# Optimization experiments

Hardware: AMD Instinct MI355X
Metric: run time of the kernel (lower is better)

## Reference

```python
import jax, jax.numpy as jnp
import numpy as np

N = 50000          # num nodes
E = 800000         # num edges (avg degree 16)
IN_C, HID_C, OUT_C = 128, 128, 64
LPA_ITER = 5


def setup_inputs() -> dict:
    key = jax.random.key(0)
    ks = jax.random.split(key, 8)
    x = jax.random.normal(ks[0], (N, IN_C), dtype=jnp.float32)
    soft_labels = jax.random.uniform(ks[1], (N, OUT_C), dtype=jnp.float32)
    edge_index = jax.random.randint(ks[2], (2, E), 0, N, dtype=jnp.int64)
    # learnable edge weights: abs() in the original, so keep them positive
    edge_attr = jax.random.uniform(ks[3], (E,), dtype=jnp.float32, minval=0.1, maxval=1.0)
    # GCNConv params (lin weight + bias)
    w1 = jax.random.normal(ks[4], (IN_C, HID_C), dtype=jnp.float32) / np.sqrt(IN_C)
    b1 = jnp.zeros((HID_C,), dtype=jnp.float32)
    w2 = jax.random.normal(ks[5], (HID_C, OUT_C), dtype=jnp.float32) / np.sqrt(HID_C)
    b2 = jnp.zeros((OUT_C,), dtype=jnp.float32)
    return {"x": x, "soft_labels": soft_labels, "edge_attr": edge_attr,
            "w1": w1, "b1": b1, "w2": w2, "b2": b2, "edge_index": edge_index}


def reference(x, soft_labels, edge_attr, w1, b1, w2, b2, edge_index):
    row, col = edge_index[0], edge_index[1]
    n = x.shape[0]
    # row-normalize the weighted sparse adjacency: A_n = D^{-1} A
    deg = jax.ops.segment_sum(edge_attr, row, num_segments=n)  # [N]
    deg_inv = jnp.where(deg == 0, 0.0, 1.0 / deg)              # inf -> 0
    val = deg_inv[row] * edge_attr                              # [E]

    def spmm(v):  # A_n @ v,  v: [N, F]
        return jax.ops.segment_sum(val[:, None] * v[col], row, num_segments=n)

    # eval mode: dropout(p=0.5, training=False) is identity
    h = jax.nn.relu(spmm(x @ w1) + b1)        # GCNConv 1 (normalize=False)
    logits = spmm(h @ w2) + b2                # GCNConv 2
    x_out = jax.nn.sigmoid(logits)

    labels = soft_labels
    for _ in range(LPA_ITER):                 # label propagation
        labels = spmm(labels)
    labels = jax.nn.sigmoid(labels)
    return (x_out, labels)
```

## Files before the change

### kernel.cpp

```cpp
#include <hip/hip_runtime.h>
#include <cstdint>
#include <cstddef>


#define WS_ALIGN(x) (((x) + 255) & ~((size_t)255))

typedef __attribute__((ext_vector_type(8))) short short8;
typedef __attribute__((ext_vector_type(4))) float floatx4;

__device__ __forceinline__ unsigned short f2bf(float f) {
    unsigned u = __float_as_uint(f);
    u += 0x7fffu + ((u >> 16) & 1u);
    return (unsigned short)(u >> 16);
}
__device__ __forceinline__ float bf_lo(unsigned u) { return __uint_as_float(u << 16); }
__device__ __forceinline__ float bf_hi(unsigned u) { return __uint_as_float(u & 0xffff0000u); }
__device__ __forceinline__ float bf2f(unsigned short h) {
    return __uint_as_float(((unsigned)h) << 16);
}
__device__ __forceinline__ unsigned pack_bf2(float a, float b) {
    return (unsigned)f2bf(a) | ((unsigned)f2bf(b) << 16);
}
__device__ __forceinline__ float sigmoidf(float x) {
    return 1.f / (1.f + __expf(-x));
}
__device__ __forceinline__ int2 ld_nt_int2(const int2* p) {
    long long v = __builtin_nontemporal_load((const long long*)p);
    int2 r;
    r.x = (int)(unsigned)(v & 0xffffffffLL);
    r.y = (int)(v >> 32);
    return r;
}

static const int NBLK = 256;
#define MAXNB 256

__launch_bounds__(256)
__global__ void binA_count(const int* __restrict__ row, int* __restrict__ bucket_count,
                           int* __restrict__ bases, int E, int chunk, int NB)
{
    __shared__ int hist[MAXNB];
    const int t = threadIdx.x;
    const int blk = blockIdx.x;
    if (t < NB) hist[t] = 0;
    __syncthreads();
    const int s = blk * chunk;
    const int e = min(E, s + chunk);
    for (int i = s + t; i < e; i += 256)
        atomicAdd(&hist[row[i] >> 8], 1);
    __syncthreads();
    if (t < NB)
        bases[blk * NB + t] = atomicAdd(&bucket_count[t], hist[t]);
}

__launch_bounds__(256)
__global__ void bin_scan(const int* __restrict__ bucket_count, int* __restrict__ bucket_start,
                         int NB)
{
    __shared__ int s[256];
    const int t = threadIdx.x;
    int v = (t < NB) ? bucket_count[t] : 0;
    s[t] = v;
    __syncthreads();
    for (int off = 1; off < 256; off <<= 1) {
        int u = (t >= off) ? s[t - off] : 0;
        __syncthreads();
        s[t] += u;
        __syncthreads();
    }
    int excl = s[t] - v;
    if (t <= NB) bucket_start[t] = excl;
}

__launch_bounds__(256)
__global__ void binA_scatter(const int* __restrict__ row, const int* __restrict__ colv,
                             const float* __restrict__ ea,
                             const int* __restrict__ bucket_start, const int* __restrict__ bases,
                             int2* __restrict__ bk, int E, int chunk, int NB)
{
    __shared__ int cur[MAXNB];
    const int t = threadIdx.x;
    const int blk = blockIdx.x;
    if (t < NB) cur[t] = bucket_start[t] + bases[blk * NB + t];
    __syncthreads();
    const int s = blk * chunk;
    const int e = min(E, s + chunk);
    for (int i = s + t; i < e; i += 256) {
        int r = row[i];
        int bin = r >> 8;
        int pos = atomicAdd(&cur[bin], 1);
        bk[pos] = make_int2(((r & 255) << 16) | colv[i], __float_as_int(ea[i]));
    }
}

__launch_bounds__(256)
__global__ void binB(const int2* __restrict__ bk, const int* __restrict__ bucket_start,
                     int* __restrict__ rowptr, int2* __restrict__ edges, int N)
{
    __shared__ int cnt[256];
    __shared__ float deg[256];
    __shared__ float inv[256];
    __shared__ int excl_s[256];
    __shared__ int cur[256];
    __shared__ int scantmp[256];
    const int b = blockIdx.x;
    const int t = threadIdx.x;
    const int s = bucket_start[b];
    const int e = bucket_start[b + 1];
    cnt[t] = 0;
    deg[t] = 0.f;
    __syncthreads();
    for (int i = s + t; i < e; i += 256) {
        int2 v = bk[i];
        int rl = ((unsigned)v.x) >> 16;
        atomicAdd(&cnt[rl], 1);
        atomicAdd(&deg[rl], __int_as_float(v.y));
    }
    __syncthreads();
    const int myc = cnt[t];
    scantmp[t] = myc;
    __syncthreads();
    for (int off = 1; off < 256; off <<= 1) {
        int u = (t >= off) ? scantmp[t - off] : 0;
        __syncthreads();
        scantmp[t] += u;
        __syncthreads();
    }
    const int excl = scantmp[t] - myc;
    excl_s[t] = excl;
    float d = deg[t];
    inv[t] = (d > 0.f) ? 1.f / d : 0.f;
    cur[t] = 0;
    const int gr = b * 256 + t;
    if (gr <= N) rowptr[gr] = s + excl;
    __syncthreads();
    for (int i = s + t; i < e; i += 256) {
        int2 v = bk[i];
        int rl = ((unsigned)v.x) >> 16;
        int c = v.x & 0xffff;
        int p = s + excl_s[rl] + atomicAdd(&cur[rl], 1);
        edges[p] = make_int2(c, __float_as_int(__int_as_float(v.y) * inv[rl]));
    }
}

__global__ void f32_to_bf16_kernel(const float* __restrict__ in, unsigned short* __restrict__ out,
                                   int n2)
{
    int i = blockIdx.x * 256 + threadIdx.x;
    if (i < n2) {
        float2 v = ((const float2*)in)[i];
        ((unsigned*)out)[i] = pack_bf2(v.x, v.y);
    }
}

template<int COLS>
__global__ void pack_w_kernel(const float* __restrict__ W, unsigned short* __restrict__ Wp)
{
    const int total = (COLS / 16) * 4 * 64;
    int idx = blockIdx.x * 256 + threadIdx.x;
    if (idx >= total) return;
    const int l = idx & 63;
    const int t = (idx >> 6) & 3;
    const int ct = idx >> 8;
    const int kbase = t * 32 + (l >> 4) * 8;
    const int col = ct * 16 + (l & 15);
    unsigned short v[8];
#pragma unroll
    for (int j = 0; j < 8; ++j)
        v[j] = f2bf(W[(size_t)(kbase + j) * COLS + col]);
    uint4 o;
    o.x = (unsigned)v[0] | ((unsigned)v[1] << 16);
    o.y = (unsigned)v[2] | ((unsigned)v[3] << 16);
    o.z = (unsigned)v[4] | ((unsigned)v[5] << 16);
    o.w = (unsigned)v[6] | ((unsigned)v[7] << 16);
    *(uint4*)(Wp + (size_t)idx * 8) = o;
}

template<int COLS>
__launch_bounds__(256)
__global__ void gemm_mfma_f32a(const float* __restrict__ A,
                               const unsigned short* __restrict__ Wp,
                               unsigned short* __restrict__ C, int M)
{
    const int wave = threadIdx.x >> 6;
    const int lane = threadIdx.x & 63;
    const int row0 = blockIdx.x * 64 + wave * 16;
    const int m = lane & 15;
    const int q = lane >> 4;

    const int arow = row0 + m;
    const bool avalid = arow < M;
    short8 a[4];
#pragma unroll
    for (int t = 0; t < 4; ++t) {
        if (avalid) {
            float4 f0 = *(const float4*)(A + (size_t)arow * 128 + t * 32 + q * 8);
            float4 f1 = *(const float4*)(A + (size_t)arow * 128 + t * 32 + q * 8 + 4);
            a[t][0] = (short)f2bf(f0.x); a[t][1] = (short)f2bf(f0.y);
            a[t][2] = (short)f2bf(f0.z); a[t][3] = (short)f2bf(f0.w);
            a[t][4] = (short)f2bf(f1.x); a[t][5] = (short)f2bf(f1.y);
            a[t][6] = (short)f2bf(f1.z); a[t][7] = (short)f2bf(f1.w);
        } else {
            a[t] = (short8)0;
        }
    }

#pragma unroll
    for (int ct = 0; ct < COLS / 16; ++ct) {
        floatx4 acc = {0.f, 0.f, 0.f, 0.f};
#pragma unroll
        for (int t = 0; t < 4; ++t) {
            short8 b = *(const short8*)(Wp + (size_t)((ct * 4 + t) * 64 + lane) * 8);
            acc = __builtin_amdgcn_mfma_f32_16x16x32_bf16(a[t], b, acc, 0, 0, 0);
        }
        const int col = ct * 16 + m;
#pragma unroll
        for (int r = 0; r < 4; ++r) {
            int orow = row0 + q * 4 + r;
            if (orow < M)
                C[(size_t)orow * COLS + col] = f2bf(acc[r]);
        }
    }
}

template<int COLS>
__launch_bounds__(256)
__global__ void gemm_mfma(const unsigned short* __restrict__ A,
                          const unsigned short* __restrict__ Wp,
                          unsigned short* __restrict__ C, int M)
{
    const int wave = threadIdx.x >> 6;
    const int lane = threadIdx.x & 63;
    const int row0 = blockIdx.x * 64 + wave * 16;
    const int m = lane & 15;
    const int q = lane >> 4;

    const int arow = row0 + m;
    const bool avalid = arow < M;
    short8 a[4];
#pragma unroll
    for (int t = 0; t < 4; ++t) {
        if (avalid)
            a[t] = *(const short8*)(A + (size_t)arow * 128 + t * 32 + q * 8);
        else
            a[t] = (short8)0;
    }

#pragma unroll
    for (int ct = 0; ct < COLS / 16; ++ct) {
        floatx4 acc = {0.f, 0.f, 0.f, 0.f};
#pragma unroll
        for (int t = 0; t < 4; ++t) {
            short8 b = *(const short8*)(Wp + (size_t)((ct * 4 + t) * 64 + lane) * 8);
            acc = __builtin_amdgcn_mfma_f32_16x16x32_bf16(a[t], b, acc, 0, 0, 0);
        }
        const int col = ct * 16 + m;
#pragma unroll
        for (int r = 0; r < 4; ++r) {
            int orow = row0 + q * 4 + r;
            if (orow < M)
                C[(size_t)orow * COLS + col] = f2bf(acc[r]);
        }
    }
}

__launch_bounds__(256)
__global__ void fused1_pair(const int* __restrict__ rowptr, const int2* __restrict__ edges,
                            const uint2* __restrict__ srcA,
                            const unsigned* __restrict__ srcB,
                            const float* __restrict__ bias,
                            uint2* __restrict__ outA,
                            unsigned* __restrict__ outB,
                            int n)
{
    const int row = blockIdx.x * 4 + (threadIdx.x >> 6);
    const int lane = threadIdx.x & 63;
    const int f = lane & 31;
    const int half = lane >> 5;
    if (row >= n) return;
    const int s = rowptr[row];
    const int e = rowptr[row + 1];

    float a0[4], a1[4], b0[2], b1[2];
#pragma unroll
    for (int j = 0; j < 4; ++j) { a0[j] = 0.f; a1[j] = 0.f; }
    b0[0] = b0[1] = b1[0] = b1[1] = 0.f;

    int i = s;
    for (; i + 8 <= e; i += 8) {
        int2 ed[4]; uint2 ua[4]; unsigned ub[4];
#pragma unroll
        for (int j = 0; j < 4; ++j) ed[j] = ld_nt_int2(&edges[i + 2 * j + half]);
#pragma unroll
        for (int j = 0; j < 4; ++j) ua[j] = srcA[(size_t)ed[j].x * 32 + f];
#pragma unroll
        for (int j = 0; j < 4; ++j) ub[j] = srcB[(size_t)ed[j].x * 32 + f];
#pragma unroll
        for (int j = 0; j < 4; ++j) {
            float w = __int_as_float(ed[j].y);
            float* A = (j & 1) ? a1 : a0;
            float* B = (j & 1) ? b1 : b0;
            A[0] = fmaf(w, bf_lo(ua[j].x), A[0]);
            A[1] = fmaf(w, bf_hi(ua[j].x), A[1]);
            A[2] = fmaf(w, bf_lo(ua[j].y), A[2]);
            A[3] = fmaf(w, bf_hi(ua[j].y), A[3]);
            B[0] = fmaf(w, bf_lo(ub[j]), B[0]);
            B[1] = fmaf(w, bf_hi(ub[j]), B[1]);
        }
    }
    for (; i + 2 <= e; i += 2) {
        int2 ed = ld_nt_int2(&edges[i + half]);
        float w = __int_as_float(ed.y);
        uint2 ua = srcA[(size_t)ed.x * 32 + f];
        unsigned ub = srcB[(size_t)ed.x * 32 + f];
        a0[0] = fmaf(w, bf_lo(ua.x), a0[0]);
        a0[1] = fmaf(w, bf_hi(ua.x), a0[1]);
        a0[2] = fmaf(w, bf_lo(ua.y), a0[2]);
        a0[3] = fmaf(w, bf_hi(ua.y), a0[3]);
        b0[0] = fmaf(w, bf_lo(ub), b0[0]);
        b0[1] = fmaf(w, bf_hi(ub), b0[1]);
    }
    if (i < e && half == 0) {
        int2 ed = ld_nt_int2(&edges[i]);
        float w = __int_as_float(ed.y);
        uint2 ua = srcA[(size_t)ed.x * 32 + f];
        unsigned ub = srcB[(size_t)ed.x * 32 + f];
        a1[0] = fmaf(w, bf_lo(ua.x), a1[0]);
        a1[1] = fmaf(w, bf_hi(ua.x), a1[1]);
        a1[2] = fmaf(w, bf_lo(ua.y), a1[2]);
        a1[3] = fmaf(w, bf_hi(ua.y), a1[3]);
        b1[0] = fmaf(w, bf_lo(ub), b1[0]);
        b1[1] = fmaf(w, bf_hi(ub), b1[1]);
    }
    float A0 = a0[0] + a1[0], A1 = a0[1] + a1[1];
    float A2 = a0[2] + a1[2], A3 = a0[3] + a1[3];
    float B0 = b0[0] + b1[0], B1 = b0[1] + b1[1];
    A0 += __shfl_down(A0, 32); A1 += __shfl_down(A1, 32);
    A2 += __shfl_down(A2, 32); A3 += __shfl_down(A3, 32);
    B0 += __shfl_down(B0, 32); B1 += __shfl_down(B1, 32);
    if (half == 0) {
        float4 bb = *(const float4*)(bias + 4 * f);
        A0 = fmaxf(A0 + bb.x, 0.f);
        A1 = fmaxf(A1 + bb.y, 0.f);
        A2 = fmaxf(A2 + bb.z, 0.f);
        A3 = fmaxf(A3 + bb.w, 0.f);
        uint2 o;
        o.x = pack_bf2(A0, A1);
        o.y = pack_bf2(A2, A3);
        outA[(size_t)row * 32 + f] = o;
        outB[(size_t)row * 32 + f] = pack_bf2(B0, B1);
    }
}

__launch_bounds__(256)
__global__ void fused2_pair(const int* __restrict__ rowptr, const int2* __restrict__ edges,
                            const unsigned* __restrict__ srcA,
                            const unsigned* __restrict__ srcB,
                            const float* __restrict__ bias,
                            float* __restrict__ outA,
                            unsigned* __restrict__ outB,
                            int n)
{
    const int row = blockIdx.x * 4 + (threadIdx.x >> 6);
    const int lane = threadIdx.x & 63;
    const int f = lane & 31;
    const int half = lane >> 5;
    if (row >= n) return;
    const int s = rowptr[row];
    const int e = rowptr[row + 1];

    float a0[2], a1[2], b0[2], b1[2];
    a0[0] = a0[1] = a1[0] = a1[1] = 0.f;
    b0[0] = b0[1] = b1[0] = b1[1] = 0.f;

    int i = s;
    for (; i + 8 <= e; i += 8) {
        int2 ed[4]; unsigned ua[4], ub[4];
#pragma unroll
        for (int j = 0; j < 4; ++j) ed[j] = ld_nt_int2(&edges[i + 2 * j + half]);
#pragma unroll
        for (int j = 0; j < 4; ++j) ua[j] = srcA[(size_t)ed[j].x * 32 + f];
#pragma unroll
        for (int j = 0; j < 4; ++j) ub[j] = srcB[(size_t)ed[j].x * 32 + f];
#pragma unroll
        for (int j = 0; j < 4; ++j) {
            float w = __int_as_float(ed[j].y);
            float* A = (j & 1) ? a1 : a0;
            float* B = (j & 1) ? b1 : b0;
            A[0] = fmaf(w, bf_lo(ua[j]), A[0]);
            A[1] = fmaf(w, bf_hi(ua[j]), A[1]);
            B[0] = fmaf(w, bf_lo(ub[j]), B[0]);
            B[1] = fmaf(w, bf_hi(ub[j]), B[1]);
        }
    }
    for (; i + 2 <= e; i += 2) {
        int2 ed = ld_nt_int2(&edges[i + half]);
        float w = __int_as_float(ed.y);
        unsigned ua = srcA[(size_t)ed.x * 32 + f];
        unsigned ub = srcB[(size_t)ed.x * 32 + f];
        a0[0] = fmaf(w, bf_lo(ua), a0[0]);
        a0[1] = fmaf(w, bf_hi(ua), a0[1]);
        b0[0] = fmaf(w, bf_lo(ub), b0[0]);
        b0[1] = fmaf(w, bf_hi(ub), b0[1]);
    }
    if (i < e && half == 0) {
        int2 ed = ld_nt_int2(&edges[i]);
        float w = __int_as_float(ed.y);
        unsigned ua = srcA[(size_t)ed.x * 32 + f];
        unsigned ub = srcB[(size_t)ed.x * 32 + f];
        a1[0] = fmaf(w, bf_lo(ua), a1[0]);
        a1[1] = fmaf(w, bf_hi(ua), a1[1]);
        b1[0] = fmaf(w, bf_lo(ub), b1[0]);
        b1[1] = fmaf(w, bf_hi(ub), b1[1]);
    }
    float A0 = a0[0] + a1[0], A1 = a0[1] + a1[1];
    float B0 = b0[0] + b1[0], B1 = b0[1] + b1[1];
    A0 += __shfl_down(A0, 32); A1 += __shfl_down(A1, 32);
    B0 += __shfl_down(B0, 32); B1 += __shfl_down(B1, 32);
    if (half == 0) {
        float2 bb = *(const float2*)(bias + 2 * f);
        float2 o;
        o.x = sigmoidf(A0 + bb.x);
        o.y = sigmoidf(A1 + bb.y);
        *(float2*)(outA + (size_t)row * 64 + 2 * f) = o;
        outB[(size_t)row * 32 + f] = pack_bf2(B0, B1);
    }
}

template<int ACT>
__launch_bounds__(256)
__global__ void spmm64_pair(const int* __restrict__ rowptr, const int2* __restrict__ edges,
                            const unsigned* __restrict__ src,
                            void* __restrict__ out, int n)
{
    const int row = blockIdx.x * 4 + (threadIdx.x >> 6);
    const int lane = threadIdx.x & 63;
    const int f = lane & 31;
    const int half = lane >> 5;
    if (row >= n) return;
    const int s = rowptr[row];
    const int e = rowptr[row + 1];

    float a[4][2];
#pragma unroll
    for (int j = 0; j < 4; ++j) { a[j][0] = 0.f; a[j][1] = 0.f; }

    int i = s;
    for (; i + 8 <= e; i += 8) {
        int2 ed[4]; unsigned u[4];
#pragma unroll
        for (int j = 0; j < 4; ++j) ed[j] = ld_nt_int2(&edges[i + 2 * j + half]);
#pragma unroll
        for (int j = 0; j < 4; ++j) u[j] = src[(size_t)ed[j].x * 32 + f];
#pragma unroll
        for (int j = 0; j < 4; ++j) {
            float w = __int_as_float(ed[j].y);
            a[j][0] = fmaf(w, bf_lo(u[j]), a[j][0]);
            a[j][1] = fmaf(w, bf_hi(u[j]), a[j][1]);
        }
    }
    for (; i + 2 <= e; i += 2) {
        int2 ed = ld_nt_int2(&edges[i + half]);
        float w = __int_as_float(ed.y);
        unsigned u = src[(size_t)ed.x * 32 + f];
        a[0][0] = fmaf(w, bf_lo(u), a[0][0]);
        a[0][1] = fmaf(w, bf_hi(u), a[0][1]);
    }
    if (i < e && half == 0) {
        int2 ed = ld_nt_int2(&edges[i]);
        float w = __int_as_float(ed.y);
        unsigned u = src[(size_t)ed.x * 32 + f];
        a[1][0] = fmaf(w, bf_lo(u), a[1][0]);
        a[1][1] = fmaf(w, bf_hi(u), a[1][1]);
    }
    float v0 = (a[0][0] + a[1][0]) + (a[2][0] + a[3][0]);
    float v1 = (a[0][1] + a[1][1]) + (a[2][1] + a[3][1]);
    v0 += __shfl_down(v0, 32);
    v1 += __shfl_down(v1, 32);
    if (half == 0) {
        if (ACT == 0) {
            ((unsigned*)out)[(size_t)row * 32 + f] = pack_bf2(v0, v1);
        } else {
            float2 o;
            o.x = sigmoidf(v0);
            o.y = sigmoidf(v1);
            *(float2*)((float*)out + (size_t)row * 64 + 2 * f) = o;
        }
    }
}

extern "C" void kernel_launch(void* const* d_in, const int* in_sizes, int n_in,
                              void* d_out, int out_size, void* d_ws, size_t ws_size,
                              hipStream_t stream)
{
    const float* x    = (const float*)d_in[0];
    const float* soft = (const float*)d_in[1];
    const float* ea   = (const float*)d_in[2];
    const float* w1   = (const float*)d_in[3];
    const float* b1   = (const float*)d_in[4];
    const float* w2   = (const float*)d_in[5];
    const float* b2   = (const float*)d_in[6];
    const int*   eidx = (const int*)d_in[7];

    const int N = in_sizes[0] / 128;
    const int E = in_sizes[2];
    const int* row  = eidx;
    const int* colv = eidx + E;
    const int NB = (N + 255) / 256;
    const int chunk = (E + NBLK - 1) / NBLK;

    uint8_t* ws = (uint8_t*)d_ws;
    size_t off = 0;
    auto alloc = [&](size_t bytes) -> void* {
        void* p = ws + off;
        off += WS_ALIGN(bytes);
        return p;
    };
    int*  bucket_count = (int*) alloc((size_t)NB * 4);
    int*  bucket_start = (int*) alloc(((size_t)NB + 1) * 4);
    int*  bases        = (int*) alloc((size_t)NBLK * NB * 4);
    int*  rowptr       = (int*) alloc(((size_t)N + 1) * 4);
    int2* bk           = (int2*)alloc((size_t)E * 8);
    int2* edges        = (int2*)alloc((size_t)E * 8);
    unsigned short* w1p     = (unsigned short*)alloc((size_t)128 * 128 * 2);
    unsigned short* w2p     = (unsigned short*)alloc((size_t)128 * 64 * 2);
    unsigned short* xw1b    = (unsigned short*)alloc((size_t)N * 128 * 2);
    unsigned short* hb      = (unsigned short*)alloc((size_t)N * 128 * 2);
    unsigned short* logitsb = (unsigned short*)alloc((size_t)N * 64 * 2);
    unsigned short* softb   = (unsigned short*)alloc((size_t)N * 64 * 2);
    unsigned short* labA    = (unsigned short*)alloc((size_t)N * 64 * 2);
    unsigned short* labB    = (unsigned short*)alloc((size_t)N * 64 * 2);

    float* out0 = (float*)d_out;
    float* out1 = out0 + (size_t)N * 64;

    hipMemsetAsync(bucket_count, 0, (size_t)NB * 4, stream);

    binA_count<<<NBLK, 256, 0, stream>>>(row, bucket_count, bases, E, chunk, NB);
    bin_scan<<<1, 256, 0, stream>>>(bucket_count, bucket_start, NB);
    binA_scatter<<<NBLK, 256, 0, stream>>>(row, colv, ea, bucket_start, bases, bk, E, chunk, NB);
    binB<<<NB, 256, 0, stream>>>(bk, bucket_start, rowptr, edges, N);

    const int ns2 = (N * 64) / 2;
    f32_to_bf16_kernel<<<(ns2 + 255) / 256, 256, 0, stream>>>(soft, softb, ns2);
    pack_w_kernel<128><<<8, 256, 0, stream>>>(w1, w1p);
    pack_w_kernel<64><<<4, 256, 0, stream>>>(w2, w2p);

    const int gGemm = (N + 63) / 64;
    const int gSp   = (N + 3) / 4;

    gemm_mfma_f32a<128><<<gGemm, 256, 0, stream>>>(x, w1p, xw1b, N);

    fused1_pair<<<gSp, 256, 0, stream>>>(rowptr, edges, (const uint2*)xw1b,
                                         (const unsigned*)softb, b1,
                                         (uint2*)hb, (unsigned*)labA, N);

    gemm_mfma<64><<<gGemm, 256, 0, stream>>>(hb, w2p, logitsb, N);

    fused2_pair<<<gSp, 256, 0, stream>>>(rowptr, edges, (const unsigned*)logitsb,
                                         (const unsigned*)labA, b2,
                                         out0, (unsigned*)labB, N);

    spmm64_pair<0><<<gSp, 256, 0, stream>>>(rowptr, edges, (const unsigned*)labB, labA, N);
    spmm64_pair<0><<<gSp, 256, 0, stream>>>(rowptr, edges, (const unsigned*)labA, labB, N);
    spmm64_pair<3><<<gSp, 256, 0, stream>>>(rowptr, edges, (const unsigned*)labB, out1, N);
}
```

Measured before the change: 317.8 us.

## Split each row's wave into four edge lanes with wider gathers and merge prep kernels

The SpMM kernels now split each 64-lane wave into four 16-lane groups, each handling a different edge. Each lane gathers 8 or 16 bytes per feature row instead of 4 or 8, and each group loads two edges with a single 16-byte nontemporal load. Partial sums are reduced with two xor-shuffles. This is meant to cut the number of gather instructions and raise memory-level parallelism per wave, at the cost of more registers and extra shuffle work. The three small prep launches (soft-label bf16 conversion and the two weight packs) are merged into one kernel to save launch overhead. The edge buffer gets padding so the paired load cannot read past the end.

Measured after the change: 323.2 us. No clear change (+1.7%).

```diff
diff --git a/kernel.cpp b/kernel.cpp
--- a/kernel.cpp
+++ b/kernel.cpp
@@ -7,6 +7,7 @@
 
 typedef __attribute__((ext_vector_type(8))) short short8;
 typedef __attribute__((ext_vector_type(4))) float floatx4;
+typedef __attribute__((ext_vector_type(4))) int intx4;
 
 __device__ __forceinline__ unsigned short f2bf(float f) {
     unsigned u = __float_as_uint(f);
@@ -15,9 +16,6 @@
 }
 __device__ __forceinline__ float bf_lo(unsigned u) { return __uint_as_float(u << 16); }
 __device__ __forceinline__ float bf_hi(unsigned u) { return __uint_as_float(u & 0xffff0000u); }
-__device__ __forceinline__ float bf2f(unsigned short h) {
-    return __uint_as_float(((unsigned)h) << 16);
-}
 __device__ __forceinline__ unsigned pack_bf2(float a, float b) {
     return (unsigned)f2bf(a) | ((unsigned)f2bf(b) << 16);
 }
@@ -30,6 +28,10 @@
     r.x = (int)(unsigned)(v & 0xffffffffLL);
     r.y = (int)(v >> 32);
     return r;
+}
+struct __attribute__((packed, aligned(8))) intx4_a8 { intx4 v; };
+__device__ __forceinline__ intx4 ld_nt_edge2(const int2* p) {
+    return __builtin_nontemporal_load(&((const intx4_a8*)p)->v);
 }
 
 static const int NBLK = 256;
@@ -143,21 +145,11 @@
     }
 }
 
-__global__ void f32_to_bf16_kernel(const float* __restrict__ in, unsigned short* __restrict__ out,
-                                   int n2)
-{
-    int i = blockIdx.x * 256 + threadIdx.x;
-    if (i < n2) {
-        float2 v = ((const float2*)in)[i];
-        ((unsigned*)out)[i] = pack_bf2(v.x, v.y);
-    }
-}
-
 template<int COLS>
-__global__ void pack_w_kernel(const float* __restrict__ W, unsigned short* __restrict__ Wp)
+__device__ __forceinline__ void pack_w_body(const float* __restrict__ W,
+                                            unsigned short* __restrict__ Wp, int idx)
 {
     const int total = (COLS / 16) * 4 * 64;
-    int idx = blockIdx.x * 256 + threadIdx.x;
     if (idx >= total) return;
     const int l = idx & 63;
     const int t = (idx >> 6) & 3;
@@ -174,6 +166,27 @@
     o.z = (unsigned)v[4] | ((unsigned)v[5] << 16);
     o.w = (unsigned)v[6] | ((unsigned)v[7] << 16);
     *(uint4*)(Wp + (size_t)idx * 8) = o;
+}
+
+__launch_bounds__(256)
+__global__ void prep_kernel(const float* __restrict__ soft, unsigned short* __restrict__ softb,
+                            int ns2,
+                            const float* __restrict__ w1, unsigned short* __restrict__ w1p,
+                            const float* __restrict__ w2, unsigned short* __restrict__ w2p)
+{
+    const int b = blockIdx.x;
+    const int t = threadIdx.x;
+    if (b < 8) {
+        pack_w_body<128>(w1, w1p, b * 256 + t);
+    } else if (b < 12) {
+        pack_w_body<64>(w2, w2p, (b - 8) * 256 + t);
+    } else {
+        int i = (b - 12) * 256 + t;
+        if (i < ns2) {
+            float2 v = ((const float2*)soft)[i];
+            ((unsigned*)softb)[i] = pack_bf2(v.x, v.y);
+        }
+    }
 }
 
 template<int COLS>
@@ -265,226 +278,240 @@
 }
 
 __launch_bounds__(256)
-__global__ void fused1_pair(const int* __restrict__ rowptr, const int2* __restrict__ edges,
-                            const uint2* __restrict__ srcA,
-                            const unsigned* __restrict__ srcB,
+__global__ void fused1_quad(const int* __restrict__ rowptr, const int2* __restrict__ edges,
+                            const uint4* __restrict__ srcA,
+                            const uint2* __restrict__ srcB,
                             const float* __restrict__ bias,
-                            uint2* __restrict__ outA,
-                            unsigned* __restrict__ outB,
+                            uint4* __restrict__ outA,
+                            uint2* __restrict__ outB,
                             int n)
 {
     const int row = blockIdx.x * 4 + (threadIdx.x >> 6);
     const int lane = threadIdx.x & 63;
-    const int f = lane & 31;
-    const int half = lane >> 5;
+    const int f = lane & 15;
+    const int q = lane >> 4;
     if (row >= n) return;
     const int s = rowptr[row];
     const int e = rowptr[row + 1];
 
-    float a0[4], a1[4], b0[2], b1[2];
-#pragma unroll
-    for (int j = 0; j < 4; ++j) { a0[j] = 0.f; a1[j] = 0.f; }
-    b0[0] = b0[1] = b1[0] = b1[1] = 0.f;
+    float A0[8], A1[8], B0[4], B1[4];
+#pragma unroll
+    for (int k = 0; k < 8; ++k) { A0[k] = 0.f; A1[k] = 0.f; }
+#pragma unroll
+    for (int k = 0; k < 4; ++k) { B0[k] = 0.f; B1[k] = 0.f; }
 
     int i = s;
     for (; i + 8 <= e; i += 8) {
-        int2 ed[4]; uint2 ua[4]; unsigned ub[4];
-#pragma unroll
-        for (int j = 0; j < 4; ++j) ed[j] = ld_nt_int2(&edges[i + 2 * j + half]);
-#pragma unroll
-        for (int j = 0; j < 4; ++j) ua[j] = srcA[(size_t)ed[j].x * 32 + f];
-#pragma unroll
-        for (int j = 0; j < 4; ++j) ub[j] = srcB[(size_t)ed[j].x * 32 + f];
-#pragma unroll
-        for (int j = 0; j < 4; ++j) {
-            float w = __int_as_float(ed[j].y);
-            float* A = (j & 1) ? a1 : a0;
-            float* B = (j & 1) ? b1 : b0;
-            A[0] = fmaf(w, bf_lo(ua[j].x), A[0]);
-            A[1] = fmaf(w, bf_hi(ua[j].x), A[1]);
-            A[2] = fmaf(w, bf_lo(ua[j].y), A[2]);
-            A[3] = fmaf(w, bf_hi(ua[j].y), A[3]);
-            B[0] = fmaf(w, bf_lo(ub[j]), B[0]);
-            B[1] = fmaf(w, bf_hi(ub[j]), B[1]);
-        }
-    }
-    for (; i + 2 <= e; i += 2) {
-        int2 ed = ld_nt_int2(&edges[i + half]);
-        float w = __int_as_float(ed.y);
-        uint2 ua = srcA[(size_t)ed.x * 32 + f];
-        unsigned ub = srcB[(size_t)ed.x * 32 + f];
-        a0[0] = fmaf(w, bf_lo(ua.x), a0[0]);
-        a0[1] = fmaf(w, bf_hi(ua.x), a0[1]);
-        a0[2] = fmaf(w, bf_lo(ua.y), a0[2]);
-        a0[3] = fmaf(w, bf_hi(ua.y), a0[3]);
-        b0[0] = fmaf(w, bf_lo(ub), b0[0]);
-        b0[1] = fmaf(w, bf_hi(ub), b0[1]);
-    }
-    if (i < e && half == 0) {
-        int2 ed = ld_nt_int2(&edges[i]);
-        float w = __int_as_float(ed.y);
-        uint2 ua = srcA[(size_t)ed.x * 32 + f];
-        unsigned ub = srcB[(size_t)ed.x * 32 + f];
-        a1[0] = fmaf(w, bf_lo(ua.x), a1[0]);
-        a1[1] = fmaf(w, bf_hi(ua.x), a1[1]);
-        a1[2] = fmaf(w, bf_lo(ua.y), a1[2]);
-        a1[3] = fmaf(w, bf_hi(ua.y), a1[3]);
-        b1[0] = fmaf(w, bf_lo(ub), b1[0]);
-        b1[1] = fmaf(w, bf_hi(ub), b1[1]);
-    }
-    float A0 = a0[0] + a1[0], A1 = a0[1] + a1[1];
-    float A2 = a0[2] + a1[2], A3 = a0[3] + a1[3];
-    float B0 = b0[0] + b1[0], B1 = b0[1] + b1[1];
-    A0 += __shfl_down(A0, 32); A1 += __shfl_down(A1, 32);
-    A2 += __shfl_down(A2, 32); A3 += __shfl_down(A3, 32);
-    B0 += __shfl_down(B0, 32); B1 += __shfl_down(B1, 32);
-    if (half == 0) {
-        float4 bb = *(const float4*)(bias + 4 * f);
-        A0 = fmaxf(A0 + bb.x, 0.f);
-        A1 = fmaxf(A1 + bb.y, 0.f);
-        A2 = fmaxf(A2 + bb.z, 0.f);
-        A3 = fmaxf(A3 + bb.w, 0.f);
-        uint2 o;
-        o.x = pack_bf2(A0, A1);
-        o.y = pack_bf2(A2, A3);
-        outA[(size_t)row * 32 + f] = o;
-        outB[(size_t)row * 32 + f] = pack_bf2(B0, B1);
-    }
-}
-
-__launch_bounds__(256)
-__global__ void fused2_pair(const int* __restrict__ rowptr, const int2* __restrict__ edges,
-                            const unsigned* __restrict__ srcA,
-                            const unsigned* __restrict__ srcB,
+        intx4 ed = ld_nt_edge2(&edges[i + 2 * q]);
+        int c0 = ed.x, c1 = ed.z;
+        float wg0 = __int_as_float(ed.y);
+        float wg1 = __int_as_float(ed.w);
+        uint4 ua0 = srcA[c0 * 16 + f];
+        uint4 ua1 = srcA[c1 * 16 + f];
+        uint2 ub0 = srcB[c0 * 16 + f];
+        uint2 ub1 = srcB[c1 * 16 + f];
+        A0[0] = fmaf(wg0, bf_lo(ua0.x), A0[0]); A0[1] = fmaf(wg0, bf_hi(ua0.x), A0[1]);
+        A0[2] = fmaf(wg0, bf_lo(ua0.y), A0[2]); A0[3] = fmaf(wg0, bf_hi(ua0.y), A0[3]);
+        A0[4] = fmaf(wg0, bf_lo(ua0.z), A0[4]); A0[5] = fmaf(wg0, bf_hi(ua0.z), A0[5]);
+        A0[6] = fmaf(wg0, bf_lo(ua0.w), A0[6]); A0[7] = fmaf(wg0, bf_hi(ua0.w), A0[7]);
+        A1[0] = fmaf(wg1, bf_lo(ua1.x), A1[0]); A1[1] = fmaf(wg1, bf_hi(ua1.x), A1[1]);
+        A1[2] = fmaf(wg1, bf_lo(ua1.y), A1[2]); A1[3] = fmaf(wg1, bf_hi(ua1.y), A1[3]);
+        A1[4] = fmaf(wg1, bf_lo(ua1.z), A1[4]); A1[5] = fmaf(wg1, bf_hi(ua1.z), A1[5]);
+        A1[6] = fmaf(wg1, bf_lo(ua1.w), A1[6]); A1[7] = fmaf(wg1, bf_hi(ua1.w), A1[7]);
+        B0[0] = fmaf(wg0, bf_lo(ub0.x), B0[0]); B0[1] = fmaf(wg0, bf_hi(ub0.x), B0[1]);
+        B0[2] = fmaf(wg0, bf_lo(ub0.y), B0[2]); B0[3] = fmaf(wg0, bf_hi(ub0.y), B0[3]);
+        B1[0] = fmaf(wg1, bf_lo(ub1.x), B1[0]); B1[1] = fmaf(wg1, bf_hi(ub1.x), B1[1]);
+        B1[2] = fmaf(wg1, bf_lo(ub1.y), B1[2]); B1[3] = fmaf(wg1, bf_hi(ub1.y), B1[3]);
+    }
+#pragma unroll
+    for (int tslot = 0; tslot < 2; ++tslot) {
+        int idx = i + q + tslot * 4;
+        if (idx < e) {
+            int2 ed = ld_nt_int2(&edges[idx]);
+            float wg = __int_as_float(ed.y);
+            uint4 ua = srcA[ed.x * 16 + f];
+            uint2 ub = srcB[ed.x * 16 + f];
+            float* A = tslot ? A1 : A0;
+            float* B = tslot ? B1 : B0;
+            A[0] = fmaf(wg, bf_lo(ua.x), A[0]); A[1] = fmaf(wg, bf_hi(ua.x), A[1]);
+            A[2] = fmaf(wg, bf_lo(ua.y), A[2]); A[3] = fmaf(wg, bf_hi(ua.y), A[3]);
+            A[4] = fmaf(wg, bf_lo(ua.z), A[4]); A[5] = fmaf(wg, bf_hi(ua.z), A[5]);
+            A[6] = fmaf(wg, bf_lo(ua.w), A[6]); A[7] = fmaf(wg, bf_hi(ua.w), A[7]);
+            B[0] = fmaf(wg, bf_lo(ub.x), B[0]); B[1] = fmaf(wg, bf_hi(ub.x), B[1]);
+            B[2] = fmaf(wg, bf_lo(ub.y), B[2]); B[3] = fmaf(wg, bf_hi(ub.y), B[3]);
+        }
+    }
+#pragma unroll
+    for (int k = 0; k < 8; ++k) {
+        float v = A0[k] + A1[k];
+        v += __shfl_xor(v, 16);
+        v += __shfl_xor(v, 32);
+        A0[k] = v;
+    }
+#pragma unroll
+    for (int k = 0; k < 4; ++k) {
+        float v = B0[k] + B1[k];
+        v += __shfl_xor(v, 16);
+        v += __shfl_xor(v, 32);
+        B0[k] = v;
+    }
+    if (q == 0) {
+        float4 bb0 = *(const float4*)(bias + 8 * f);
+        float4 bb1 = *(const float4*)(bias + 8 * f + 4);
+        float h0 = fmaxf(A0[0] + bb0.x, 0.f), h1 = fmaxf(A0[1] + bb0.y, 0.f);
+        float h2 = fmaxf(A0[2] + bb0.z, 0.f), h3 = fmaxf(A0[3] + bb0.w, 0.f);
+        float h4 = fmaxf(A0[4] + bb1.x, 0.f), h5 = fmaxf(A0[5] + bb1.y, 0.f);
+        float h6 = fmaxf(A0[6] + bb1.z, 0.f), h7 = fmaxf(A0[7] + bb1.w, 0.f);
+        uint4 o;
+        o.x = pack_bf2(h0, h1);
+        o.y = pack_bf2(h2, h3);
+        o.z = pack_bf2(h4, h5);
+        o.w = pack_bf2(h6, h7);
+        outA[row * 16 + f] = o;
+        outB[row * 16 + f] = make_uint2(pack_bf2(B0[0], B0[1]), pack_bf2(B0[2], B0[3]));
+    }
+}
+
+__launch_bounds__(256)
+__global__ void fused2_quad(const int* __restrict__ rowptr, const int2* __restrict__ edges,
+                            const uint2* __restrict__ srcA,
+                            const uint2* __restrict__ srcB,
                             const float* __restrict__ bias,
                             float* __restrict__ outA,
-                            unsigned* __restrict__ outB,
+                            uint2* __restrict__ outB,
                             int n)
 {
     const int row = blockIdx.x * 4 + (threadIdx.x >> 6);
     const int lane = threadIdx.x & 63;
-    const int f = lane & 31;
-    const int half = lane >> 5;
+    const int f = lane & 15;
+    const int q = lane >> 4;
     if (row >= n) return;
     const int s = rowptr[row];
     const int e = rowptr[row + 1];
 
-    float a0[2], a1[2], b0[2], b1[2];
-    a0[0] = a0[1] = a1[0] = a1[1] = 0.f;
-    b0[0] = b0[1] = b1[0] = b1[1] = 0.f;
+    float A0[4], A1[4], B0[4], B1[4];
+#pragma unroll
+    for (int k = 0; k < 4; ++k) { A0[k] = 0.f; A1[k] = 0.f; B0[k] = 0.f; B1[k] = 0.f; }
 
     int i = s;
     for (; i + 8 <= e; i += 8) {
-        int2 ed[4]; unsigned ua[4], ub[4];
-#pragma unroll
-        for (int j = 0; j < 4; ++j) ed[j] = ld_nt_int2(&edges[i + 2 * j + half]);
-#pragma unroll
-        for (int j = 0; j < 4; ++j) ua[j] = srcA[(size_t)ed[j].x * 32 + f];
-#pragma unroll
-        for (int j = 0; j < 4; ++j) ub[j] = srcB[(size_t)ed[j].x * 32 + f];
-#pragma unroll
-        for (int j = 0; j < 4; ++j) {
-            float w = __int_as_float(ed[j].y);
-            float* A = (j & 1) ? a1 : a0;
-            float* B = (j & 1) ? b1 : b0;
-            A[0] = fmaf(w, bf_lo(ua[j]), A[0]);
-            A[1] = fmaf(w, bf_hi(ua[j]), A[1]);
-            B[0] = fmaf(w, bf_lo(ub[j]), B[0]);
-            B[1] = fmaf(w, bf_hi(ub[j]), B[1]);
-        }
-    }
-    for (; i + 2 <= e; i += 2) {
-        int2 ed = ld_nt_int2(&edges[i + half]);
-        float w = __int_as_float(ed.y);
-        unsigned ua = srcA[(size_t)ed.x * 32 + f];
-        unsigned ub = srcB[(size_t)ed.x * 32 + f];
-        a0[0] = fmaf(w, bf_lo(ua), a0[0]);
-        a0[1] = fmaf(w, bf_hi(ua), a0[1]);
-        b0[0] = fmaf(w, bf_lo(ub), b0[0]);
-        b0[1] = fmaf(w, bf_hi(ub), b0[1]);
-    }
-    if (i < e && half == 0) {
-        int2 ed = ld_nt_int2(&edges[i]);
-        float w = __int_as_float(ed.y);
-        unsigned ua = srcA[(size_t)ed.x * 32 + f];
-        unsigned ub = srcB[(size_t)ed.x * 32 + f];
-        a1[0] = fmaf(w, bf_lo(ua), a1[0]);
-        a1[1] = fmaf(w, bf_hi(ua), a1[1]);
-        b1[0] = fmaf(w, bf_lo(ub), b1[0]);
-        b1[1] = fmaf(w, bf_hi(ub), b1[1]);
-    }
-    float A0 = a0[0] + a1[0], A1 = a0[1] + a1[1];
-    float B0 = b0[0] + b1[0], B1 = b0[1] + b1[1];
-    A0 += __shfl_down(A0, 32); A1 += __shfl_down(A1, 32);
-    B0 += __shfl_down(B0, 32); B1 += __shfl_down(B1, 32);
-    if (half == 0) {
-        float2 bb = *(const float2*)(bias + 2 * f);
-        float2 o;
-        o.x = sigmoidf(A0 + bb.x);
-        o.y = sigmoidf(A1 + bb.y);
-        *(float2*)(outA + (size_t)row * 64 + 2 * f) = o;
-        outB[(size_t)row * 32 + f] = pack_bf2(B0, B1);
+        intx4 ed = ld_nt_edge2(&edges[i + 2 * q]);
+        int c0 = ed.x, c1 = ed.z;
+        float wg0 = __int_as_float(ed.y);
+        float wg1 = __int_as_float(ed.w);
+        uint2 ua0 = srcA[c0 * 16 + f];
+        uint2 ua1 = srcA[c1 * 16 + f];
+        uint2 ub0 = srcB[c0 * 16 + f];
+        uint2 ub1 = srcB[c1 * 16 + f];
+        A0[0] = fmaf(wg0, bf_lo(ua0.x), A0[0]); A0[1] = fmaf(wg0, bf_hi(ua0.x), A0[1]);
+        A0[2] = fmaf(wg0, bf_lo(ua0.y), A0[2]); A0[3] = fmaf(wg0, bf_hi(ua0.y), A0[3]);
+        A1[0] = fmaf(wg1, bf_lo(ua1.x), A1[0]); A1[1] = fmaf(wg1, bf_hi(ua1.x), A1[1]);
+        A1[2] = fmaf(wg1, bf_lo(ua1.y), A1[2]); A1[3] = fmaf(wg1, bf_hi(ua1.y), A1[3]);
+        B0[0] = fmaf(wg0, bf_lo(ub0.x), B0[0]); B0[1] = fmaf(wg0, bf_hi(ub0.x), B0[1]);
+        B0[2] = fmaf(wg0, bf_lo(ub0.y), B0[2]); B0[3] = fmaf(wg0, bf_hi(ub0.y), B0[3]);
+        B1[0] = fmaf(wg1, bf_lo(ub1.x), B1[0]); B1[1] = fmaf(wg1, bf_hi(ub1.x), B1[1]);
+        B1[2] = fmaf(wg1, bf_lo(ub1.y), B1[2]); B1[3] = fmaf(wg1, bf_hi(ub1.y), B1[3]);
+    }
+#pragma unroll
+    for (int tslot = 0; tslot < 2; ++tslot) {
+        int idx = i + q + tslot * 4;
+        if (idx < e) {
+            int2 ed = ld_nt_int2(&edges[idx]);
+            float wg = __int_as_float(ed.y);
+            uint2 ua = srcA[ed.x * 16 + f];
+            uint2 ub = srcB[ed.x * 16 + f];
+            float* A = tslot ? A1 : A0;
+            float* B = tslot ? B1 : B0;
+            A[0] = fmaf(wg, bf_lo(ua.x), A[0]); A[1] = fmaf(wg, bf_hi(ua.x), A[1]);
+            A[2] = fmaf(wg, bf_lo(ua.y), A[2]); A[3] = fmaf(wg, bf_hi(ua.y), A[3]);
+            B[0] = fmaf(wg, bf_lo(ub.x), B[0]); B[1] = fmaf(wg, bf_hi(ub.x), B[1]);
+            B[2] = fmaf(wg, bf_lo(ub.y), B[2]); B[3] = fmaf(wg, bf_hi(ub.y), B[3]);
+        }
+    }
+#pragma unroll
+    for (int k = 0; k < 4; ++k) {
+        float v = A0[k] + A1[k];
+        v += __shfl_xor(v, 16);
+        v += __shfl_xor(v, 32);
+        A0[k] = v;
+        float u = B0[k] + B1[k];
+        u += __shfl_xor(u, 16);
+        u += __shfl_xor(u, 32);
+        B0[k] = u;
+    }
+    if (q == 0) {
+        float4 bb = *(const float4*)(bias + 4 * f);
+        float4 o;
+        o.x = sigmoidf(A0[0] + bb.x);
+        o.y = sigmoidf(A0[1] + bb.y);
+        o.z = sigmoidf(A0[2] + bb.z);
+        o.w = sigmoidf(A0[3] + bb.w);
+        *(float4*)(outA + (size_t)row * 64 + 4 * f) = o;
+        outB[row * 16 + f] = make_uint2(pack_bf2(B0[0], B0[1]), pack_bf2(B0[2], B0[3]));
     }
 }
 
 template<int ACT>
 __launch_bounds__(256)
-__global__ void spmm64_pair(const int* __restrict__ rowptr, const int2* __restrict__ edges,
-                            const unsigned* __restrict__ src,
+__global__ void spmm64_quad(const int* __restrict__ rowptr, const int2* __restrict__ edges,
+                            const uint2* __restrict__ src,
                             void* __restrict__ out, int n)
 {
     const int row = blockIdx.x * 4 + (threadIdx.x >> 6);
     const int lane = threadIdx.x & 63;
-    const int f = lane & 31;
-    const int half = lane >> 5;
+    const int f = lane & 15;
+    const int q = lane >> 4;
     if (row >= n) return;
     const int s = rowptr[row];
     const int e = rowptr[row + 1];
 
-    float a[4][2];
-#pragma unroll
-    for (int j = 0; j < 4; ++j) { a[j][0] = 0.f; a[j][1] = 0.f; }
+    float A0[4], A1[4];
+#pragma unroll
+    for (int k = 0; k < 4; ++k) { A0[k] = 0.f; A1[k] = 0.f; }
 
     int i = s;
     for (; i + 8 <= e; i += 8) {
-        int2 ed[4]; unsigned u[4];
-#pragma unroll
-        for (int j = 0; j < 4; ++j) ed[j] = ld_nt_int2(&edges[i + 2 * j + half]);
-#pragma unroll
-        for (int j = 0; j < 4; ++j) u[j] = src[(size_t)ed[j].x * 32 + f];
-#pragma unroll
-        for (int j = 0; j < 4; ++j) {
-            float w = __int_as_float(ed[j].y);
-            a[j][0] = fmaf(w, bf_lo(u[j]), a[j][0]);
-            a[j][1] = fmaf(w, bf_hi(u[j]), a[j][1]);
-        }
-    }
-    for (; i + 2 <= e; i += 2) {
-        int2 ed = ld_nt_int2(&edges[i + half]);
-        float w = __int_as_float(ed.y);
-        unsigned u = src[(size_t)ed.x * 32 + f];
-        a[0][0] = fmaf(w, bf_lo(u), a[0][0]);
-        a[0][1] = fmaf(w, bf_hi(u), a[0][1]);
-    }
-    if (i < e && half == 0) {
-        int2 ed = ld_nt_int2(&edges[i]);
-        float w = __int_as_float(ed.y);
-        unsigned u = src[(size_t)ed.x * 32 + f];
-        a[1][0] = fmaf(w, bf_lo(u), a[1][0]);
-        a[1][1] = fmaf(w, bf_hi(u), a[1][1]);
-    }
-    float v0 = (a[0][0] + a[1][0]) + (a[2][0] + a[3][0]);
-    float v1 = (a[0][1] + a[1][1]) + (a[2][1] + a[3][1]);
-    v0 += __shfl_down(v0, 32);
-    v1 += __shfl_down(v1, 32);
-    if (half == 0) {
+        intx4 ed = ld_nt_edge2(&edges[i + 2 * q]);
+        int c0 = ed.x, c1 = ed.z;
+        float wg0 = __int_as_float(ed.y);
+        float wg1 = __int_as_float(ed.w);
+        uint2 u0 = src[c0 * 16 + f];
+        uint2 u1 = src[c1 * 16 + f];
+        A0[0] = fmaf(wg0, bf_lo(u0.x), A0[0]); A0[1] = fmaf(wg0, bf_hi(u0.x), A0[1]);
+        A0[2] = fmaf(wg0, bf_lo(u0.y), A0[2]); A0[3] = fmaf(wg0, bf_hi(u0.y), A0[3]);
+        A1[0] = fmaf(wg1, bf_lo(u1.x), A1[0]); A1[1] = fmaf(wg1, bf_hi(u1.x), A1[1]);
+        A1[2] = fmaf(wg1, bf_lo(u1.y), A1[2]); A1[3] = fmaf(wg1, bf_hi(u1.y), A1[3]);
+    }
+#pragma unroll
+    for (int tslot = 0; tslot < 2; ++tslot) {
+        int idx = i + q + tslot * 4;
+        if (idx < e) {
+            int2 ed = ld_nt_int2(&edges[idx]);
+            float wg = __int_as_float(ed.y);
+            uint2 u = src[ed.x * 16 + f];
+            float* A = tslot ? A1 : A0;
+            A[0] = fmaf(wg, bf_lo(u.x), A[0]); A[1] = fmaf(wg, bf_hi(u.x), A[1]);
+            A[2] = fmaf(wg, bf_lo(u.y), A[2]); A[3] = fmaf(wg, bf_hi(u.y), A[3]);
+        }
+    }
+#pragma unroll
+    for (int k = 0; k < 4; ++k) {
+        float v = A0[k] + A1[k];
+        v += __shfl_xor(v, 16);
+        v += __shfl_xor(v, 32);
+        A0[k] = v;
+    }
+    if (q == 0) {
         if (ACT == 0) {
-            ((unsigned*)out)[(size_t)row * 32 + f] = pack_bf2(v0, v1);
+            ((uint2*)out)[row * 16 + f] =
+                make_uint2(pack_bf2(A0[0], A0[1]), pack_bf2(A0[2], A0[3]));
         } else {
-            float2 o;
-            o.x = sigmoidf(v0);
-            o.y = sigmoidf(v1);
-            *(float2*)((float*)out + (size_t)row * 64 + 2 * f) = o;
+            float4 o;
+            o.x = sigmoidf(A0[0]);
+            o.y = sigmoidf(A0[1]);
+            o.z = sigmoidf(A0[2]);
+            o.w = sigmoidf(A0[3]);
+            *(float4*)((float*)out + (size_t)row * 64 + 4 * f) = o;
         }
     }
 }
@@ -521,7 +548,7 @@
     int*  bases        = (int*) alloc((size_t)NBLK * NB * 4);
     int*  rowptr       = (int*) alloc(((size_t)N + 1) * 4);
     int2* bk           = (int2*)alloc((size_t)E * 8);
-    int2* edges        = (int2*)alloc((size_t)E * 8);
+    int2* edges        = (int2*)alloc((size_t)E * 8 + 64);
     unsigned short* w1p     = (unsigned short*)alloc((size_t)128 * 128 * 2);
     unsigned short* w2p     = (unsigned short*)alloc((size_t)128 * 64 * 2);
     unsigned short* xw1b    = (unsigned short*)alloc((size_t)N * 128 * 2);
@@ -542,26 +569,25 @@
     binB<<<NB, 256, 0, stream>>>(bk, bucket_start, rowptr, edges, N);
 
     const int ns2 = (N * 64) / 2;
-    f32_to_bf16_kernel<<<(ns2 + 255) / 256, 256, 0, stream>>>(soft, softb, ns2);
-    pack_w_kernel<128><<<8, 256, 0, stream>>>(w1, w1p);
-    pack_w_kernel<64><<<4, 256, 0, stream>>>(w2, w2p);
+    const int gPrep = 12 + (ns2 + 255) / 256;
+    prep_kernel<<<gPrep, 256, 0, stream>>>(soft, softb, ns2, w1, w1p, w2, w2p);
 
     const int gGemm = (N + 63) / 64;
     const int gSp   = (N + 3) / 4;
 
     gemm_mfma_f32a<128><<<gGemm, 256, 0, stream>>>(x, w1p, xw1b, N);
 
-    fused1_pair<<<gSp, 256, 0, stream>>>(rowptr, edges, (const uint2*)xw1b,
-                                         (const unsigned*)softb, b1,
-                                         (uint2*)hb, (unsigned*)labA, N);
+    fused1_quad<<<gSp, 256, 0, stream>>>(rowptr, edges, (const uint4*)xw1b,
+                                         (const uint2*)softb, b1,
+                                         (uint4*)hb, (uint2*)labA, N);
 
     gemm_mfma<64><<<gGemm, 256, 0, stream>>>(hb, w2p, logitsb, N);
 
-    fused2_pair<<<gSp, 256, 0, stream>>>(rowptr, edges, (const unsigned*)logitsb,
-                                         (const unsigned*)labA, b2,
-                                         out0, (unsigned*)labB, N);
-
-    spmm64_pair<0><<<gSp, 256, 0, stream>>>(rowptr, edges, (const unsigned*)labB, labA, N);
-    spmm64_pair<0><<<gSp, 256, 0, stream>>>(rowptr, edges, (const unsigned*)labA, labB, N);
-    spmm64_pair<3><<<gSp, 256, 0, stream>>>(rowptr, edges, (const unsigned*)labB, out1, N);
-}
+    fused2_quad<<<gSp, 256, 0, stream>>>(rowptr, edges, (const uint2*)logitsb,
+                                         (const uint2*)labA, b2,
+                                         out0, (uint2*)labB, N);
+
+    spmm64_quad<0><<<gSp, 256, 0, stream>>>(rowptr, edges, (const uint2*)labB, labA, N);
+    spmm64_quad<0><<<gSp, 256, 0, stream>>>(rowptr, edges, (const uint2*)labA, labB, N);
+    spmm64_quad<3><<<gSp, 256, 0, stream>>>(rowptr, edges, (const uint2*)labB, out1, N);
+}
```

## Merge preprocessing launches into combined kernels and co-schedule GEMM with edge scatter

Applied to the files above, without the earlier changes.

Combines the bucket-count pass, the weight packing and the soft-label bf16 conversion into one launch, using block-index ranges to pick the work. Also merges the first dense GEMM with the edge-bucket scatter so the two independent jobs share one grid and can overlap. This cuts launch count and fills the idle gaps left by the small kernels. The trade-off is heterogeneous blocks sharing one launch-bounds setting and one shared-memory footprint, which may cost occupancy. The edges buffer also gets a little padding.

After: 306.9 us (median of 2 runs). -3.4%, faster.

```diff
diff --git a/kernel.cpp b/kernel.cpp
--- a/kernel.cpp
+++ b/kernel.cpp
@@ -15,9 +15,6 @@
 }
 __device__ __forceinline__ float bf_lo(unsigned u) { return __uint_as_float(u << 16); }
 __device__ __forceinline__ float bf_hi(unsigned u) { return __uint_as_float(u & 0xffff0000u); }
-__device__ __forceinline__ float bf2f(unsigned short h) {
-    return __uint_as_float(((unsigned)h) << 16);
-}
 __device__ __forceinline__ unsigned pack_bf2(float a, float b) {
     return (unsigned)f2bf(a) | ((unsigned)f2bf(b) << 16);
 }
@@ -35,13 +32,13 @@
 static const int NBLK = 256;
 #define MAXNB 256
 
-__launch_bounds__(256)
-__global__ void binA_count(const int* __restrict__ row, int* __restrict__ bucket_count,
-                           int* __restrict__ bases, int E, int chunk, int NB)
+__device__ __forceinline__ void binA_count_body(const int* __restrict__ row,
+                                                int* __restrict__ bucket_count,
+                                                int* __restrict__ bases,
+                                                int E, int chunk, int NB, int blk)
 {
     __shared__ int hist[MAXNB];
     const int t = threadIdx.x;
-    const int blk = blockIdx.x;
     if (t < NB) hist[t] = 0;
     __syncthreads();
     const int s = blk * chunk;
@@ -72,15 +69,16 @@
     if (t <= NB) bucket_start[t] = excl;
 }
 
-__launch_bounds__(256)
-__global__ void binA_scatter(const int* __restrict__ row, const int* __restrict__ colv,
-                             const float* __restrict__ ea,
-                             const int* __restrict__ bucket_start, const int* __restrict__ bases,
-                             int2* __restrict__ bk, int E, int chunk, int NB)
+__device__ __forceinline__ void binA_scatter_body(const int* __restrict__ row,
+                                                  const int* __restrict__ colv,
+                                                  const float* __restrict__ ea,
+                                                  const int* __restrict__ bucket_start,
+                                                  const int* __restrict__ bases,
+                                                  int2* __restrict__ bk,
+                                                  int E, int chunk, int NB, int blk)
 {
     __shared__ int cur[MAXNB];
     const int t = threadIdx.x;
-    const int blk = blockIdx.x;
     if (t < NB) cur[t] = bucket_start[t] + bases[blk * NB + t];
     __syncthreads();
     const int s = blk * chunk;
@@ -143,21 +141,11 @@
     }
 }
 
-__global__ void f32_to_bf16_kernel(const float* __restrict__ in, unsigned short* __restrict__ out,
-                                   int n2)
-{
-    int i = blockIdx.x * 256 + threadIdx.x;
-    if (i < n2) {
-        float2 v = ((const float2*)in)[i];
-        ((unsigned*)out)[i] = pack_bf2(v.x, v.y);
-    }
-}
-
 template<int COLS>
-__global__ void pack_w_kernel(const float* __restrict__ W, unsigned short* __restrict__ Wp)
+__device__ __forceinline__ void pack_w_body(const float* __restrict__ W,
+                                            unsigned short* __restrict__ Wp, int idx)
 {
     const int total = (COLS / 16) * 4 * 64;
-    int idx = blockIdx.x * 256 + threadIdx.x;
     if (idx >= total) return;
     const int l = idx & 63;
     const int t = (idx >> 6) & 3;
@@ -176,15 +164,42 @@
     *(uint4*)(Wp + (size_t)idx * 8) = o;
 }
 
-template<int COLS>
-__launch_bounds__(256)
-__global__ void gemm_mfma_f32a(const float* __restrict__ A,
-                               const unsigned short* __restrict__ Wp,
-                               unsigned short* __restrict__ C, int M)
-{
+__launch_bounds__(256)
+__global__ void count_prep(const int* __restrict__ row, int* __restrict__ bucket_count,
+                           int* __restrict__ bases, int E, int chunk, int NB,
+                           const float* __restrict__ soft, unsigned short* __restrict__ softb,
+                           int ns2,
+                           const float* __restrict__ w1, unsigned short* __restrict__ w1p,
+                           const float* __restrict__ w2, unsigned short* __restrict__ w2p)
+{
+    const int b = blockIdx.x;
+    const int t = threadIdx.x;
+    if (b < NBLK) {
+        binA_count_body(row, bucket_count, bases, E, chunk, NB, b);
+    } else {
+        const int bb = b - NBLK;
+        if (bb < 8) {
+            pack_w_body<128>(w1, w1p, bb * 256 + t);
+        } else if (bb < 12) {
+            pack_w_body<64>(w2, w2p, (bb - 8) * 256 + t);
+        } else {
+            int i = (bb - 12) * 256 + t;
+            if (i < ns2) {
+                float2 v = ((const float2*)soft)[i];
+                ((unsigned*)softb)[i] = pack_bf2(v.x, v.y);
+            }
+        }
+    }
+}
+
+__device__ __forceinline__ void gemm128_f32a_body(const float* __restrict__ A,
+                                                  const unsigned short* __restrict__ Wp,
+                                                  unsigned short* __restrict__ C, int M, int bid)
+{
+    const int COLS = 128;
     const int wave = threadIdx.x >> 6;
     const int lane = threadIdx.x & 63;
-    const int row0 = blockIdx.x * 64 + wave * 16;
+    const int row0 = bid * 64 + wave * 16;
     const int m = lane & 15;
     const int q = lane >> 4;
 
@@ -220,6 +235,22 @@
             if (orow < M)
                 C[(size_t)orow * COLS + col] = f2bf(acc[r]);
         }
+    }
+}
+
+__launch_bounds__(256)
+__global__ void gemm_scatter(const float* __restrict__ A, const unsigned short* __restrict__ Wp,
+                             unsigned short* __restrict__ C, int M, int gGemm,
+                             const int* __restrict__ row, const int* __restrict__ colv,
+                             const float* __restrict__ ea,
+                             const int* __restrict__ bucket_start, const int* __restrict__ bases,
+                             int2* __restrict__ bk, int E, int chunk, int NB)
+{
+    const int b = blockIdx.x;
+    if (b < gGemm) {
+        gemm128_f32a_body(A, Wp, C, M, b);
+    } else {
+        binA_scatter_body(row, colv, ea, bucket_start, bases, bk, E, chunk, NB, b - gGemm);
     }
 }
 
@@ -521,7 +552,7 @@
     int*  bases        = (int*) alloc((size_t)NBLK * NB * 4);
     int*  rowptr       = (int*) alloc(((size_t)N + 1) * 4);
     int2* bk           = (int2*)alloc((size_t)E * 8);
-    int2* edges        = (int2*)alloc((size_t)E * 8);
+    int2* edges        = (int2*)alloc((size_t)E * 8 + 64);
     unsigned short* w1p     = (unsigned short*)alloc((size_t)128 * 128 * 2);
     unsigned short* w2p     = (unsigned short*)alloc((size_t)128 * 64 * 2);
     unsigned short* xw1b    = (unsigned short*)alloc((size_t)N * 128 * 2);
@@ -536,20 +567,21 @@
 
     hipMemsetAsync(bucket_count, 0, (size_t)NB * 4, stream);
 
-    binA_count<<<NBLK, 256, 0, stream>>>(row, bucket_count, bases, E, chunk, NB);
-    bin_scan<<<1, 256, 0, stream>>>(bucket_count, bucket_start, NB);
-    binA_scatter<<<NBLK, 256, 0, stream>>>(row, colv, ea, bucket_start, bases, bk, E, chunk, NB);
-    binB<<<NB, 256, 0, stream>>>(bk, bucket_start, rowptr, edges, N);
-
     const int ns2 = (N * 64) / 2;
-    f32_to_bf16_kernel<<<(ns2 + 255) / 256, 256, 0, stream>>>(soft, softb, ns2);
-    pack_w_kernel<128><<<8, 256, 0, stream>>>(w1, w1p);
-    pack_w_kernel<64><<<4, 256, 0, stream>>>(w2, w2p);
-
     const int gGemm = (N + 63) / 64;
     const int gSp   = (N + 3) / 4;
 
-    gemm_mfma_f32a<128><<<gGemm, 256, 0, stream>>>(x, w1p, xw1b, N);
+    const int gCP = NBLK + 12 + (ns2 + 255) / 256;
+    count_prep<<<gCP, 256, 0, stream>>>(row, bucket_count, bases, E, chunk, NB,
+                                        soft, softb, ns2, w1, w1p, w2, w2p);
+
+    bin_scan<<<1, 256, 0, stream>>>(bucket_count, bucket_start, NB);
+
+    gemm_scatter<<<gGemm + NBLK, 256, 0, stream>>>(x, w1p, xw1b, N, gGemm,
+                                                   row, colv, ea, bucket_start, bases,
+                                                   bk, E, chunk, NB);
+
+    binB<<<NB, 256, 0, stream>>>(bk, bucket_start, rowptr, edges, N);
 
     fused1_pair<<<gSp, 256, 0, stream>>>(rowptr, edges, (const uint2*)xw1b,
                                          (const unsigned*)softb, b1,
```
